# Kernel optimization log

Hardware: AMD Instinct MI355X
Metric: run time of the kernel (lower is better)

The kernel has to match this reference:

```python
import jax, jax.numpy as jnp
import numpy as np

B, S, H, F, E, K = 4, 2048, 1024, 3584, 8, 2
CAP_FACTOR = 1.25


def setup_inputs() -> dict:
    key = jax.random.key(0)
    k1, k2, k3, k4, k5 = jax.random.split(key, 5)
    s_h = 1.0 / np.sqrt(H)
    s_f = 1.0 / np.sqrt(F)
    return {
        "hidden_states": jax.random.normal(k1, (B, S, H), dtype=jnp.float32),
        "gate_w": jax.random.normal(k2, (E, H), dtype=jnp.float32) * s_h,
        "w1": jax.random.normal(k3, (E, H, F), dtype=jnp.float32) * s_h,
        "w2": jax.random.normal(k4, (E, F, H), dtype=jnp.float32) * s_f,
        "w3": jax.random.normal(k5, (E, H, F), dtype=jnp.float32) * s_h,
    }


def _moe_forward(hidden_states, gate_w, w1, w2, w3):
    b, s, h = hidden_states.shape
    dtype = hidden_states.dtype
    x = hidden_states.reshape(-1, h)  # [B*S, H]
    router_logits = x @ gate_w.T  # [B*S, E]
    expert_weights = jax.nn.softmax(router_logits.astype(jnp.float32), axis=1)
    _, selected_experts = jax.lax.top_k(expert_weights, K)  # [B*S, K]

    top_k_idx = selected_experts.reshape(b, s, K)
    probs = expert_weights.reshape(b, s, E)

    capacity = int(s * K / E * CAP_FACTOR)  # expert capacity per batch

    # dispatch/combine masks (Mixtral 'dropping' implementation)
    expert_mask = jax.nn.one_hot(top_k_idx, E, dtype=jnp.int32)  # [b,s,K,E]
    mask_fused = expert_mask.reshape(b, s * K, E)
    count_fused = jnp.cumsum(mask_fused, axis=1)  # running count per expert
    count = count_fused.reshape(b, s, K, E)
    trunc_mask = expert_mask * (count <= capacity).astype(jnp.int32)
    combined_mask = trunc_mask.sum(axis=2)  # [b,s,E]
    masked_probs = probs * combined_mask  # drop over-capacity tokens

    pos_fused = mask_fused * count_fused
    pos = pos_fused.reshape(b, s, K, E)
    combined_pos = pos.sum(axis=2) * combined_mask  # [b,s,E], 1-based slot
    pos_in_cap = jax.nn.one_hot(combined_pos, capacity + 1, dtype=jnp.int32)
    combine_mask = masked_probs[..., None] * pos_in_cap  # [b,s,E,cap+1]
    combine_mask = combine_mask[..., 1:].astype(dtype)  # drop slot 0 (dropped tokens)
    dispatch_mask = (combine_mask != 0).astype(dtype)  # [b,s,E,cap]

    # dispatch tokens into per-expert capacity buffers
    dispatch = jnp.einsum('bsm,bsec->ebcm', hidden_states, dispatch_mask)
    # expert FFN (SwiGLU)
    h1 = jnp.einsum('ebcm,emh->ebch', dispatch, w1)
    h3 = jnp.einsum('ebcm,emh->ebch', dispatch, w3)
    expert_out = jnp.einsum('ebch,ehm->ebcm', jax.nn.silu(h1) * h3, w2)
    # combine back to token order with routing probabilities
    final = jnp.einsum('ebcm,bsec->bsm', expert_out, combine_mask)
    return final


def reference(hidden_states, gate_w, w1, w2, w3):
    return _moe_forward(hidden_states, gate_w, w1, w2, w3)
```

## Files before the change

### kernel.cpp

```cpp
#include <hip/hip_runtime.h>
#include <hip/hip_bf16.h>
#include <math.h>

#define B_   4
#define S_   2048
#define H_   1024
#define F_   3584
#define E_   8
#define TOPK 2
#define CAP  640
#define M_   (B_*CAP)
#define NTOK (B_*S_)

typedef __attribute__((ext_vector_type(8))) short short8;
typedef __attribute__((ext_vector_type(4))) float f32x4;
typedef __attribute__((ext_vector_type(4))) unsigned short us4;

static __device__ __forceinline__ unsigned short f2bf(float f) {
  __hip_bfloat16 h = __float2bfloat16(f);
  return *reinterpret_cast<unsigned short*>(&h);
}
static __device__ __forceinline__ float bf2f(unsigned short u) {
  unsigned int x = ((unsigned int)u) << 16;
  float f;
  __builtin_memcpy(&f, &x, 4);
  return f;
}

static __device__ __forceinline__ void gload16(const void* g, void* l) {
  __builtin_amdgcn_global_load_lds((const __attribute__((address_space(1))) void*)g,
                                   (__attribute__((address_space(3))) void*)l, 16, 0, 0);
}

#define BAR() __builtin_amdgcn_s_barrier()
#define SCB() __builtin_amdgcn_sched_barrier(0)
#define WLG() asm volatile("s_waitcnt lgkmcnt(0)" ::: "memory")
#define WLG4() asm volatile("s_waitcnt lgkmcnt(4)" ::: "memory")
#define VM4() asm volatile("s_waitcnt vmcnt(4)" ::: "memory")
#define VM0() asm volatile("s_waitcnt vmcnt(0)" ::: "memory")

__global__ __launch_bounds__(64) void k_router(const float* __restrict__ hs,
                                               const float* __restrict__ gw,
                                               int* __restrict__ e01,
                                               float* __restrict__ p01) {
  int t = blockIdx.x;
  int lane = threadIdx.x;
  const float4* xv = (const float4*)(hs + (size_t)t * H_);
  float4 xr[4];
#pragma unroll
  for (int i = 0; i < 4; ++i) xr[i] = xv[lane + i * 64];
  float logit[E_];
#pragma unroll
  for (int e = 0; e < E_; ++e) {
    const float4* gv = (const float4*)(gw + (size_t)e * H_);
    float acc = 0.f;
#pragma unroll
    for (int i = 0; i < 4; ++i) {
      float4 g = gv[lane + i * 64];
      acc += xr[i].x * g.x + xr[i].y * g.y + xr[i].z * g.z + xr[i].w * g.w;
    }
#pragma unroll
    for (int off = 32; off > 0; off >>= 1) acc += __shfl_xor(acc, off);
    logit[e] = acc;
  }
  float mx = logit[0];
#pragma unroll
  for (int e = 1; e < E_; ++e) mx = fmaxf(mx, logit[e]);
  float p[E_], s = 0.f;
#pragma unroll
  for (int e = 0; e < E_; ++e) { p[e] = expf(logit[e] - mx); s += p[e]; }
  float inv = 1.f / s;
  int e0 = 0;
#pragma unroll
  for (int e = 1; e < E_; ++e) if (p[e] > p[e0]) e0 = e;
  int e1 = (e0 == 0) ? 1 : 0;
#pragma unroll
  for (int e = 0; e < E_; ++e) if (e != e0 && p[e] > p[e1]) e1 = e;
  if (lane == 0) {
    e01[t * 2 + 0] = e0;
    e01[t * 2 + 1] = e1;
    p01[t * 2 + 0] = p[e0] * inv;
    p01[t * 2 + 1] = p[e1] * inv;
  }
}

__global__ __launch_bounds__(256) void k_positions(const int* __restrict__ e01,
                                                   int* __restrict__ pos,
                                                   int* __restrict__ disp) {
  int b = blockIdx.x, tid = threadIdx.x;
  __shared__ unsigned char eid[S_ * TOPK];
  __shared__ int part[256];
  for (int i = tid; i < E_ * CAP; i += 256)
    disp[((size_t)(i / CAP) * B_ + b) * CAP + (i % CAP)] = -1;
  for (int i = tid; i < S_ * TOPK; i += 256)
    eid[i] = (unsigned char)e01[b * S_ * TOPK + i];
  __syncthreads();
  const int per = (S_ * TOPK) / 256;
  int base = tid * per;
  for (int e = 0; e < E_; ++e) {
    int cnt = 0;
    for (int j = 0; j < per; ++j) cnt += (eid[base + j] == e) ? 1 : 0;
    part[tid] = cnt;
    __syncthreads();
    for (int off = 1; off < 256; off <<= 1) {
      int v = part[tid];
      int add = (tid >= off) ? part[tid - off] : 0;
      __syncthreads();
      part[tid] = v + add;
      __syncthreads();
    }
    int run = part[tid] - cnt;
    for (int j = 0; j < per; ++j) {
      int sl = base + j;
      if (eid[sl] == e) {
        ++run;
        int p = (run <= CAP) ? (run - 1) : -1;
        pos[b * S_ * TOPK + sl] = p;
        if (p >= 0) disp[((size_t)e * B_ + b) * CAP + p] = sl >> 1;
      }
    }
    __syncthreads();
  }
}

__global__ __launch_bounds__(256) void k_transpose(const float* __restrict__ in,
                                                   unsigned short* __restrict__ outp,
                                                   int R, int C, int ileave, int half,
                                                   size_t ostride_e) {
  __shared__ unsigned short ls[64][72];
  int e = blockIdx.z, tc = blockIdx.x, tr = blockIdx.y, tid = threadIdx.x;
  const float* src = in + (size_t)e * R * C + (size_t)tr * 64 * C + (size_t)tc * 64;
#pragma unroll
  for (int i = 0; i < 16; ++i) {
    int row = i * 4 + (tid >> 6), col = tid & 63;
    ls[row][col] = f2bf(src[(size_t)row * C + col]);
  }
  __syncthreads();
  unsigned short* dbase = outp + (size_t)e * ostride_e;
#pragma unroll
  for (int i = 0; i < 4; ++i) {
    int orow = i * 16 + (tid >> 4), oc = (tid & 15) * 4;
    int gr = tc * 64 + orow;
    int ri = ileave ? ((gr & ~15) * 2 + (gr & 15) + half * 16) : gr;
    us4 v = {ls[oc + 0][orow], ls[oc + 1][orow], ls[oc + 2][orow], ls[oc + 3][orow]};
    *(us4*)&dbase[(size_t)ri * R + tr * 64 + oc] = v;
  }
}

__global__ __launch_bounds__(256) void k_dispatch(const float* __restrict__ hs,
                                                  const int* __restrict__ disp,
                                                  unsigned short* __restrict__ xd) {
  int slot = blockIdx.x;
  int tid = threadIdx.x;
  int tok = disp[slot];
  int b = (slot / CAP) % B_;
  us4 v;
  if (tok >= 0) {
    const float4* src = (const float4*)(hs + ((size_t)b * S_ + tok) * H_);
    float4 f = src[tid];
    v = {f2bf(f.x), f2bf(f.y), f2bf(f.z), f2bf(f.w)};
  } else {
    v = {0, 0, 0, 0};
  }
  *(us4*)&xd[(size_t)slot * H_ + tid * 4] = v;
}

#define STAGE_A(d, h, t) {                                                    \
    const unsigned short* _p = srcA + (size_t)(t) * 64 + (h) * 32;            \
    gload16(_p, &lds[((d) * 2 + (h)) * 8192 + tid * 8]);                      \
    gload16(_p + (size_t)128 * KTOT, &lds[((d) * 2 + (h)) * 8192 + tid * 8 + 4096]); \
  }
#define STAGE_B(d, h, t) {                                                    \
    const unsigned short* _p = srcB + (size_t)(t) * 64 + (h) * 32;            \
    gload16(_p, &lds[32768 + ((d) * 2 + (h)) * 8192 + tid * 8]);              \
    gload16(_p + (size_t)128 * KTOT, &lds[32768 + ((d) * 2 + (h)) * 8192 + tid * 8 + 4096]); \
  }
#define RD_A4(d, h, mh) {                                                     \
    const unsigned short* _pa = &lds[((d) * 2 + (h)) * 8192 + aoff + (mh) * 2048]; \
    _Pragma("unroll") for (int j = 0; j < 4; ++j)                             \
      a[j] = *(const short8*)&_pa[j * 512];                                   \
  }
#define RD_B4(d, h) {                                                         \
    const unsigned short* _pb = &lds[32768 + ((d) * 2 + (h)) * 8192 + boff];  \
    _Pragma("unroll") for (int n = 0; n < 4; ++n)                             \
      b[n] = *(const short8*)&_pb[n * 512];                                   \
  }
#define MFMA16(mh) {                                                          \
    __builtin_amdgcn_s_setprio(1);                                            \
    _Pragma("unroll") for (int j = 0; j < 4; ++j)                             \
      _Pragma("unroll") for (int n = 0; n < 4; ++n)                           \
        acc[(mh) * 4 + j][n] = __builtin_amdgcn_mfma_f32_16x16x32_bf16(a[j], b[n], acc[(mh) * 4 + j][n], 0, 0, 0); \
    __builtin_amdgcn_s_setprio(0);                                            \
  }
#define BODY(P, tn) {                                                         \
    RD_A4(P, 0, 0); RD_B4(P, 0); STAGE_A((P) ^ 1, 0, tn);                     \
    SCB(); WLG4(); BAR(); WLG(); SCB();                                       \
    MFMA16(0); BAR();                                                         \
    RD_A4(P, 0, 1); STAGE_B((P) ^ 1, 0, tn); VM4();                           \
    SCB(); BAR(); WLG(); SCB();                                               \
    MFMA16(1); BAR();                                                         \
    RD_A4(P, 1, 0); RD_B4(P, 1); STAGE_A((P) ^ 1, 1, tn);                     \
    SCB(); WLG4(); BAR(); WLG(); SCB();                                       \
    MFMA16(0); BAR();                                                         \
    RD_A4(P, 1, 1); STAGE_B((P) ^ 1, 1, tn); VM4();                           \
    SCB(); BAR(); WLG(); SCB();                                               \
    MFMA16(1); BAR();                                                         \
  }
#define PEEL(P) {                                                             \
    RD_A4(P, 0, 0); RD_B4(P, 0);                                              \
    SCB(); WLG4(); BAR(); WLG(); SCB();                                       \
    MFMA16(0); BAR();                                                         \
    RD_A4(P, 0, 1); VM0();                                                    \
    SCB(); BAR(); WLG(); SCB();                                               \
    MFMA16(1); BAR();                                                         \
    RD_A4(P, 1, 0); RD_B4(P, 1);                                              \
    SCB(); WLG4(); BAR(); WLG(); SCB();                                       \
    MFMA16(0); BAR();                                                         \
    RD_A4(P, 1, 1);                                                           \
    SCB(); BAR(); WLG(); SCB();                                               \
    MFMA16(1);                                                                \
  }

template <int KTOT, bool SWIGLU, int MT, int NTN, int NTOTB, int SPLITK>
__global__ __launch_bounds__(512, 2) void k_gemm256(const unsigned short* __restrict__ Aall,
                                                    const unsigned short* __restrict__ Ball,
                                                    unsigned short* __restrict__ Cout) {
  constexpr int KSUB = KTOT / SPLITK;
  constexpr int NT = KSUB / 64;
  __shared__ __align__(16) unsigned short lds[65536];

  const int nwg = MT * NTN * E_ * SPLITK;
  int lid = blockIdx.x;
  int sw = (lid & 7) * (nwg >> 3) + (lid >> 3);
  constexpr int PER = MT * NTN;
  int ks = sw / (PER * E_);
  int rem2 = sw - ks * (PER * E_);
  int e = rem2 / PER;
  int rem = rem2 - e * PER;
  int tn = rem / MT, tm = rem - tn * MT;

  int tid = threadIdx.x, li = tid & 63, wid = tid >> 6;
  int wm = wid >> 2, wn = wid & 3;

  int rS = tid >> 2;
  int gS = (tid & 3) ^ ((tid >> 3) & 3);
  const unsigned short* srcA = Aall + ((size_t)e * M_ + (size_t)tm * 256 + rS) * KTOT + ks * KSUB + gS * 8;
  const unsigned short* srcB = Ball + ((size_t)e * NTOTB + (size_t)tn * 256 + rS) * KTOT + ks * KSUB + gS * 8;

  int sA = (li >> 4) ^ ((li >> 1) & 3);
  int aoff = (wm * 128 + (li & 15)) * 32 + sA * 8;
  int boff = (wn * 64 + (li & 15)) * 32 + sA * 8;

  f32x4 acc[8][4] = {};
  short8 a[4], b[4];

  STAGE_A(0, 0, 0); STAGE_B(0, 0, 0);
  STAGE_A(0, 1, 0); STAGE_B(0, 1, 0);
  VM4();
  BAR();

#pragma unroll 1
  for (int t = 0; t + 1 < NT - 1; t += 2) {
    BODY(0, t + 1);
    BODY(1, t + 2);
  }
  if constexpr (((NT - 1) & 1) != 0) {
    BODY(0, NT - 1);
  }
  if constexpr (((NT - 1) & 1) != 0) {
    PEEL(1);
  } else {
    PEEL(0);
  }

  int r0 = tm * 256 + wm * 128 + ((li >> 4) << 2);
  if constexpr (SWIGLU) {
    unsigned short* out = Cout + (size_t)e * M_ * F_;
#pragma unroll
    for (int m = 0; m < 8; ++m)
#pragma unroll
      for (int u = 0; u < 2; ++u) {
        int col = (tn * 8 + wn * 2 + u) * 16 + (li & 15);
#pragma unroll
        for (int j = 0; j < 4; ++j) {
          float h1 = acc[m][2 * u][j], h3 = acc[m][2 * u + 1][j];
          float sg = 1.f / (1.f + __expf(-h1));
          out[(size_t)(r0 + m * 16 + j) * F_ + col] = f2bf(h1 * sg * h3);
        }
      }
  } else {
    unsigned short* out = Cout + ((size_t)ks * E_ + e) * M_ * NTOTB;
#pragma unroll
    for (int m = 0; m < 8; ++m)
#pragma unroll
      for (int n = 0; n < 4; ++n) {
        int col = tn * 256 + wn * 64 + n * 16 + (li & 15);
#pragma unroll
        for (int j = 0; j < 4; ++j)
          out[(size_t)(r0 + m * 16 + j) * NTOTB + col] = f2bf(acc[m][n][j]);
      }
  }
}

__global__ __launch_bounds__(256) void k_combine(const unsigned short* __restrict__ Oe0,
                                                 const unsigned short* __restrict__ Oe1,
                                                 const int* __restrict__ e01,
                                                 const float* __restrict__ p01,
                                                 const int* __restrict__ pos,
                                                 float* __restrict__ outp) {
  int t = blockIdx.x;
  int b = t / S_;
  int tid = threadIdx.x;
  float4 acc = {0.f, 0.f, 0.f, 0.f};
#pragma unroll
  for (int k = 0; k < TOPK; ++k) {
    int p = pos[t * 2 + k];
    if (p >= 0) {
      int e = e01[t * 2 + k];
      float w = p01[t * 2 + k];
      size_t row = (size_t)e * M_ + (size_t)b * CAP + p;
      us4 v0 = *(const us4*)&Oe0[row * H_ + tid * 4];
      us4 v1 = *(const us4*)&Oe1[row * H_ + tid * 4];
      acc.x += w * (bf2f(v0[0]) + bf2f(v1[0]));
      acc.y += w * (bf2f(v0[1]) + bf2f(v1[1]));
      acc.z += w * (bf2f(v0[2]) + bf2f(v1[2]));
      acc.w += w * (bf2f(v0[3]) + bf2f(v1[3]));
    }
  }
  *(float4*)&outp[(size_t)t * H_ + tid * 4] = acc;
}

extern "C" void kernel_launch(void* const* d_in, const int* in_sizes, int n_in,
                              void* d_out, int out_size, void* d_ws, size_t ws_size,
                              hipStream_t stream) {
  const float* hs = (const float*)d_in[0];
  const float* gw = (const float*)d_in[1];
  const float* w1 = (const float*)d_in[2];
  const float* w2 = (const float*)d_in[3];
  const float* w3 = (const float*)d_in[4];

  char* ws = (char*)d_ws;
  size_t off = 0;
  auto take = [&](size_t bytes) -> char* {
    char* p = ws + off;
    off += (bytes + 255) & ~(size_t)255;
    return p;
  };
  int*            e01  = (int*)take((size_t)NTOK * 2 * 4);
  float*          p01  = (float*)take((size_t)NTOK * 2 * 4);
  int*            pos  = (int*)take((size_t)NTOK * 2 * 4);
  int*            disp = (int*)take((size_t)E_ * B_ * CAP * 4);
  unsigned short* w13t = (unsigned short*)take((size_t)E_ * 2 * F_ * H_ * 2);
  unsigned short* w2t  = (unsigned short*)take((size_t)E_ * H_ * F_ * 2);
  unsigned short* xd   = (unsigned short*)take((size_t)E_ * M_ * H_ * 2);
  unsigned short* act  = (unsigned short*)take((size_t)E_ * M_ * F_ * 2);
  unsigned short* oe   = (unsigned short*)take((size_t)2 * E_ * M_ * H_ * 2);

  k_router<<<NTOK, 64, 0, stream>>>(hs, gw, e01, p01);
  k_positions<<<B_, 256, 0, stream>>>(e01, pos, disp);
  k_transpose<<<dim3(F_ / 64, H_ / 64, E_), 256, 0, stream>>>(w1, w13t, H_, F_, 1, 0, (size_t)2 * F_ * H_);
  k_transpose<<<dim3(F_ / 64, H_ / 64, E_), 256, 0, stream>>>(w3, w13t, H_, F_, 1, 1, (size_t)2 * F_ * H_);
  k_transpose<<<dim3(H_ / 64, F_ / 64, E_), 256, 0, stream>>>(w2, w2t, F_, H_, 0, 0, (size_t)H_ * F_);
  k_dispatch<<<E_ * B_ * CAP, 256, 0, stream>>>(hs, disp, xd);
  k_gemm256<H_, true, M_ / 256, (2 * F_) / 256, 2 * F_, 1>
      <<<(M_ / 256) * ((2 * F_) / 256) * E_, 512, 0, stream>>>(xd, w13t, act);
  k_gemm256<F_, false, M_ / 256, H_ / 256, H_, 2>
      <<<(M_ / 256) * (H_ / 256) * E_ * 2, 512, 0, stream>>>(act, w2t, oe);
  k_combine<<<NTOK, 256, 0, stream>>>(oe, oe + (size_t)E_ * M_ * H_, e01, p01, pos, (float*)d_out);
}
```

Baseline: 608.4 us.

## Switch expert GEMMs to 32x32x16 MFMA with matching LDS fragment layout

```diff
diff --git a/kernel.cpp b/kernel.cpp
--- a/kernel.cpp
+++ b/kernel.cpp
@@ -14,6 +14,7 @@
 
 typedef __attribute__((ext_vector_type(8))) short short8;
 typedef __attribute__((ext_vector_type(4))) float f32x4;
+typedef __attribute__((ext_vector_type(16))) float f32x16;
 typedef __attribute__((ext_vector_type(4))) unsigned short us4;
 
 static __device__ __forceinline__ unsigned short f2bf(float f) {
@@ -35,7 +36,6 @@
 #define BAR() __builtin_amdgcn_s_barrier()
 #define SCB() __builtin_amdgcn_sched_barrier(0)
 #define WLG() asm volatile("s_waitcnt lgkmcnt(0)" ::: "memory")
-#define WLG4() asm volatile("s_waitcnt lgkmcnt(4)" ::: "memory")
 #define VM4() asm volatile("s_waitcnt vmcnt(4)" ::: "memory")
 #define VM0() asm volatile("s_waitcnt vmcnt(0)" ::: "memory")
 
@@ -141,7 +141,7 @@
   for (int i = 0; i < 4; ++i) {
     int orow = i * 16 + (tid >> 4), oc = (tid & 15) * 4;
     int gr = tc * 64 + orow;
-    int ri = ileave ? ((gr & ~15) * 2 + (gr & 15) + half * 16) : gr;
+    int ri = ileave ? ((gr & ~31) * 2 + (gr & 31) + half * 32) : gr;
     us4 v = {ls[oc + 0][orow], ls[oc + 1][orow], ls[oc + 2][orow], ls[oc + 3][orow]};
     *(us4*)&dbase[(size_t)ri * R + tr * 64 + oc] = v;
   }
@@ -176,49 +176,55 @@
     gload16(_p + (size_t)128 * KTOT, &lds[32768 + ((d) * 2 + (h)) * 8192 + tid * 8 + 4096]); \
   }
 #define RD_A4(d, h, mh) {                                                     \
-    const unsigned short* _pa = &lds[((d) * 2 + (h)) * 8192 + aoff + (mh) * 2048]; \
-    _Pragma("unroll") for (int j = 0; j < 4; ++j)                             \
-      a[j] = *(const short8*)&_pa[j * 512];                                   \
+    const unsigned short* _pa = &lds[((d) * 2 + (h)) * 8192 + abase + (mh) * 2048]; \
+    a[0] = *(const short8*)&_pa[s0];                                          \
+    a[1] = *(const short8*)&_pa[s1];                                          \
+    a[2] = *(const short8*)&_pa[1024 + s0];                                   \
+    a[3] = *(const short8*)&_pa[1024 + s1];                                   \
   }
 #define RD_B4(d, h) {                                                         \
-    const unsigned short* _pb = &lds[32768 + ((d) * 2 + (h)) * 8192 + boff];  \
-    _Pragma("unroll") for (int n = 0; n < 4; ++n)                             \
-      b[n] = *(const short8*)&_pb[n * 512];                                   \
-  }
-#define MFMA16(mh) {                                                          \
+    const unsigned short* _pb = &lds[32768 + ((d) * 2 + (h)) * 8192 + bbase]; \
+    b[0] = *(const short8*)&_pb[s0];                                          \
+    b[1] = *(const short8*)&_pb[s1];                                          \
+    b[2] = *(const short8*)&_pb[1024 + s0];                                   \
+    b[3] = *(const short8*)&_pb[1024 + s1];                                   \
+  }
+#define MFMA8(mh) {                                                           \
     __builtin_amdgcn_s_setprio(1);                                            \
-    _Pragma("unroll") for (int j = 0; j < 4; ++j)                             \
-      _Pragma("unroll") for (int n = 0; n < 4; ++n)                           \
-        acc[(mh) * 4 + j][n] = __builtin_amdgcn_mfma_f32_16x16x32_bf16(a[j], b[n], acc[(mh) * 4 + j][n], 0, 0, 0); \
+    _Pragma("unroll") for (int m = 0; m < 2; ++m)                             \
+      _Pragma("unroll") for (int n = 0; n < 2; ++n) {                         \
+        acc[(mh) * 2 + m][n] = __builtin_amdgcn_mfma_f32_32x32x16_bf16(a[m * 2 + 0], b[n * 2 + 0], acc[(mh) * 2 + m][n], 0, 0, 0); \
+        acc[(mh) * 2 + m][n] = __builtin_amdgcn_mfma_f32_32x32x16_bf16(a[m * 2 + 1], b[n * 2 + 1], acc[(mh) * 2 + m][n], 0, 0, 0); \
+      }                                                                       \
     __builtin_amdgcn_s_setprio(0);                                            \
   }
 #define BODY(P, tn) {                                                         \
     RD_A4(P, 0, 0); RD_B4(P, 0); STAGE_A((P) ^ 1, 0, tn);                     \
-    SCB(); WLG4(); BAR(); WLG(); SCB();                                       \
-    MFMA16(0); BAR();                                                         \
+    SCB(); BAR(); WLG(); SCB();                                               \
+    MFMA8(0); BAR();                                                          \
     RD_A4(P, 0, 1); STAGE_B((P) ^ 1, 0, tn); VM4();                           \
     SCB(); BAR(); WLG(); SCB();                                               \
-    MFMA16(1); BAR();                                                         \
+    MFMA8(1); BAR();                                                          \
     RD_A4(P, 1, 0); RD_B4(P, 1); STAGE_A((P) ^ 1, 1, tn);                     \
-    SCB(); WLG4(); BAR(); WLG(); SCB();                                       \
-    MFMA16(0); BAR();                                                         \
+    SCB(); BAR(); WLG(); SCB();                                               \
+    MFMA8(0); BAR();                                                          \
     RD_A4(P, 1, 1); STAGE_B((P) ^ 1, 1, tn); VM4();                           \
     SCB(); BAR(); WLG(); SCB();                                               \
-    MFMA16(1); BAR();                                                         \
+    MFMA8(1); BAR();                                                          \
   }
 #define PEEL(P) {                                                             \
     RD_A4(P, 0, 0); RD_B4(P, 0);                                              \
-    SCB(); WLG4(); BAR(); WLG(); SCB();                                       \
-    MFMA16(0); BAR();                                                         \
+    SCB(); BAR(); WLG(); SCB();                                               \
+    MFMA8(0); BAR();                                                          \
     RD_A4(P, 0, 1); VM0();                                                    \
     SCB(); BAR(); WLG(); SCB();                                               \
-    MFMA16(1); BAR();                                                         \
+    MFMA8(1); BAR();                                                          \
     RD_A4(P, 1, 0); RD_B4(P, 1);                                              \
-    SCB(); WLG4(); BAR(); WLG(); SCB();                                       \
-    MFMA16(0); BAR();                                                         \
+    SCB(); BAR(); WLG(); SCB();                                               \
+    MFMA8(0); BAR();                                                          \
     RD_A4(P, 1, 1);                                                           \
     SCB(); BAR(); WLG(); SCB();                                               \
-    MFMA16(1);                                                                \
+    MFMA8(1);                                                                 \
   }
 
 template <int KTOT, bool SWIGLU, int MT, int NTN, int NTOTB, int SPLITK>
@@ -247,11 +253,15 @@
   const unsigned short* srcA = Aall + ((size_t)e * M_ + (size_t)tm * 256 + rS) * KTOT + ks * KSUB + gS * 8;
   const unsigned short* srcB = Ball + ((size_t)e * NTOTB + (size_t)tn * 256 + rS) * KTOT + ks * KSUB + gS * 8;
 
-  int sA = (li >> 4) ^ ((li >> 1) & 3);
-  int aoff = (wm * 128 + (li & 15)) * 32 + sA * 8;
-  int boff = (wn * 64 + (li & 15)) * 32 + sA * 8;
-
-  f32x4 acc[8][4] = {};
+  int lr = li & 31;
+  int ck = li >> 5;
+  int sz = (lr >> 1) & 3;
+  int abase = (wm * 128 + lr) * 32;
+  int bbase = (wn * 64 + lr) * 32;
+  int s0 = (ck ^ sz) * 8;
+  int s1 = ((ck | 2) ^ sz) * 8;
+
+  f32x16 acc[4][2] = {};
   short8 a[4], b[4];
 
   STAGE_A(0, 0, 0); STAGE_B(0, 0, 0);
@@ -273,31 +283,32 @@
     PEEL(0);
   }
 
-  int r0 = tm * 256 + wm * 128 + ((li >> 4) << 2);
+  int rbase = tm * 256 + wm * 128 + 4 * ck;
   if constexpr (SWIGLU) {
     unsigned short* out = Cout + (size_t)e * M_ * F_;
-#pragma unroll
-    for (int m = 0; m < 8; ++m)
-#pragma unroll
-      for (int u = 0; u < 2; ++u) {
-        int col = (tn * 8 + wn * 2 + u) * 16 + (li & 15);
-#pragma unroll
-        for (int j = 0; j < 4; ++j) {
-          float h1 = acc[m][2 * u][j], h3 = acc[m][2 * u + 1][j];
-          float sg = 1.f / (1.f + __expf(-h1));
-          out[(size_t)(r0 + m * 16 + j) * F_ + col] = f2bf(h1 * sg * h3);
-        }
+    int col = tn * 128 + wn * 32 + lr;
+#pragma unroll
+    for (int mf = 0; mf < 4; ++mf) {
+#pragma unroll
+      for (int reg = 0; reg < 16; ++reg) {
+        int r = rbase + mf * 32 + (reg & 3) + 8 * (reg >> 2);
+        float h1 = acc[mf][0][reg], h3 = acc[mf][1][reg];
+        float sg = 1.f / (1.f + __expf(-h1));
+        out[(size_t)r * F_ + col] = f2bf(h1 * sg * h3);
       }
+    }
   } else {
     unsigned short* out = Cout + ((size_t)ks * E_ + e) * M_ * NTOTB;
 #pragma unroll
-    for (int m = 0; m < 8; ++m)
-#pragma unroll
-      for (int n = 0; n < 4; ++n) {
-        int col = tn * 256 + wn * 64 + n * 16 + (li & 15);
-#pragma unroll
-        for (int j = 0; j < 4; ++j)
-          out[(size_t)(r0 + m * 16 + j) * NTOTB + col] = f2bf(acc[m][n][j]);
+    for (int mf = 0; mf < 4; ++mf)
+#pragma unroll
+      for (int n = 0; n < 2; ++n) {
+        int col = tn * 256 + wn * 64 + n * 32 + lr;
+#pragma unroll
+        for (int reg = 0; reg < 16; ++reg) {
+          int r = rbase + mf * 32 + (reg & 3) + 8 * (reg >> 2);
+          out[(size_t)r * NTOTB + col] = f2bf(acc[mf][n][reg]);
+        }
       }
   }
 }
```

Result: slower. 631.0 us (+3.7%).
